# Kernel optimization log

Hardware: AMD Instinct MI355X
Metric: run time of the kernel (lower is better)

Reference implementation:

```python
import jax, jax.numpy as jnp
import numpy as np
from jax import lax

NUM_HEADS = 4
SIDE = 5  # side_dwconv


def setup_inputs() -> dict:
    key = jax.random.key(0)
    ks = jax.random.split(key, 7)
    B, C, H, W = 2, 128, 56, 56
    return {
        "x": jax.random.normal(ks[0], (B, C, H, W), dtype=jnp.float32),
        "qkv_w": jax.random.normal(ks[1], (3 * C, C), dtype=jnp.float32) * 0.02,
        "qkv_b": jax.random.normal(ks[2], (3 * C,), dtype=jnp.float32) * 0.02,
        "lepe_w": jax.random.normal(ks[3], (C, 1, SIDE, SIDE), dtype=jnp.float32) * 0.02,
        "lepe_b": jax.random.normal(ks[4], (C,), dtype=jnp.float32) * 0.02,
        "proj_w": jax.random.normal(ks[5], (C, C), dtype=jnp.float32) * 0.02,
        "proj_b": jax.random.normal(ks[6], (C,), dtype=jnp.float32) * 0.02,
    }


def reference(x, qkv_w, qkv_b, lepe_w, lepe_b, proj_w, proj_b):
    B, C, H, W = x.shape
    nh = NUM_HEADS
    hd = C // nh
    scale = hd ** (-0.5)
    N = H * W

    # 1x1 conv qkv == channel matmul
    qkv = jnp.einsum('oc,bchw->bohw', qkv_w, x) + qkv_b[None, :, None, None]
    q, k, v = jnp.split(qkv, 3, axis=1)  # each [B, C, H, W]

    qr = q.reshape(B, nh, hd, N)
    kr = k.reshape(B, nh, hd, N)
    vr = v.reshape(B, nh, hd, N)

    # attn = q^T k over head_dim -> [B, nh, N, N]
    attn = jnp.einsum('bhdn,bhdm->bhnm', qr, kr) * scale
    attn = jax.nn.softmax(attn, axis=-1)

    # out = attn @ v^T, then permute back to [B, C, H, W]
    out = jnp.einsum('bhnm,bhdm->bhdn', attn, vr).reshape(B, C, H, W)

    # depthwise LePE conv on v, fused with residual add
    pad = SIDE // 2
    lepe = lax.conv_general_dilated(
        v, lepe_w, window_strides=(1, 1), padding=[(pad, pad), (pad, pad)],
        dimension_numbers=('NCHW', 'OIHW', 'NCHW'), feature_group_count=C,
    ) + lepe_b[None, :, None, None]
    out = out + lepe

    # 1x1 conv proj
    out = jnp.einsum('oc,bchw->bohw', proj_w, out) + proj_b[None, :, None, None]
    return out
```

## Files before the change

kernel.cpp:

```cpp
#include <hip/hip_runtime.h>

typedef __bf16 bf16x8 __attribute__((ext_vector_type(8)));
typedef __bf16 bf16x4 __attribute__((ext_vector_type(4)));
typedef float  f32x4  __attribute__((ext_vector_type(4)));

#define NPIX  3136
#define WIMG  56
#define CCH   128
#define NH    4
#define HD    32
#define QSCALE 0.2550565470841439f

#if __has_builtin(__builtin_amdgcn_exp2f)
#define FEXP2(x) __builtin_amdgcn_exp2f(x)
#else
#define FEXP2(x) __expf((x) * 0.6931471805599453f)
#endif


__global__ __launch_bounds__(256) void k_qkv(
    const float* __restrict__ x, const float* __restrict__ qkv_w,
    const float* __restrict__ qkv_b,
    __bf16* __restrict__ qT, __bf16* __restrict__ kT,
    __bf16* __restrict__ vT, __bf16* __restrict__ vP)
{
    __shared__ __bf16 xl[CCH][68];
    const int tid = threadIdx.x;
    const int w = tid >> 6, lane = tid & 63;
    const int col = lane & 15, g = lane >> 4;
    const int px0 = blockIdx.x * 64;
    const int oslab = blockIdx.y;
    const int b = blockIdx.z;
    const int obase = oslab * 64 + w * 16;

    {
        const int pxg = tid & 15, cb = tid >> 4;
        const float* xp = x + (size_t)b * CCH * NPIX + px0 + 4 * pxg;
        #pragma unroll
        for (int pass = 0; pass < 8; ++pass) {
            const int c = cb + 16 * pass;
            const float4 xv = *(const float4*)(xp + (size_t)c * NPIX);
            bf16x4 v = {(__bf16)xv.x, (__bf16)xv.y, (__bf16)xv.z, (__bf16)xv.w};
            *(bf16x4*)&xl[c][4 * pxg] = v;
        }
    }
    __syncthreads();

    f32x4 acc[4];
    #pragma unroll
    for (int a = 0; a < 4; ++a) acc[a] = (f32x4){0.f, 0.f, 0.f, 0.f};

    const float* wrow = qkv_w + (size_t)(obase + col) * CCH;
    #pragma unroll
    for (int ks = 0; ks < 4; ++ks) {
        const int c0 = ks * 32 + g * 8;
        bf16x8 af;
        #pragma unroll
        for (int j = 0; j < 8; ++j) af[j] = (__bf16)wrow[c0 + j];
        #pragma unroll
        for (int a = 0; a < 4; ++a) {
            bf16x8 bf_;
            #pragma unroll
            for (int j = 0; j < 8; ++j) bf_[j] = xl[c0 + j][16 * a + col];
            acc[a] = __builtin_amdgcn_mfma_f32_16x16x32_bf16(af, bf_, acc[a], 0, 0, 0);
        }
    }

    const int orow = obase + g * 4;
    const f32x4 bias4 = *(const f32x4*)(qkv_b + orow);

    if (oslab < 2) {
        const int h = orow >> 5, d0 = orow & 31;
        __bf16* dst = qT + ((size_t)(b * NH + h) * NPIX) * HD + d0;
        #pragma unroll
        for (int a = 0; a < 4; ++a) {
            const int px = px0 + 16 * a + col;
            bf16x4 v;
            #pragma unroll
            for (int r = 0; r < 4; ++r) v[r] = (__bf16)((acc[a][r] + bias4[r]) * QSCALE);
            *(bf16x4*)(dst + (size_t)px * HD) = v;
        }
    } else if (oslab < 4) {
        const int o2 = orow - 128;
        const int h = o2 >> 5, d0 = o2 & 31;
        __bf16* dst = kT + ((size_t)(b * NH + h) * NPIX) * HD + d0;
        #pragma unroll
        for (int a = 0; a < 4; ++a) {
            const int px = px0 + 16 * a + col;
            bf16x4 v;
            #pragma unroll
            for (int r = 0; r < 4; ++r) v[r] = (__bf16)(acc[a][r] + bias4[r]);
            *(bf16x4*)(dst + (size_t)px * HD) = v;
        }
    } else {
        const int c = orow - 256;
        #pragma unroll
        for (int a = 0; a < 4; ++a) {
            const int px = px0 + 16 * a + col;
            bf16x4 v;
            #pragma unroll
            for (int r = 0; r < 4; ++r) v[r] = (__bf16)(acc[a][r] + bias4[r]);
            *(bf16x4*)(vT + ((size_t)(b * NPIX + px)) * CCH + c) = v;
            const int sp = px0 + 4 * col + a;
            #pragma unroll
            for (int r = 0; r < 4; ++r)
                vP[((size_t)(b * CCH + c + r)) * NPIX + sp] = v[r];
        }
    }
}

__global__ __launch_bounds__(256) void k_attn(
    const __bf16* __restrict__ qT, const __bf16* __restrict__ kT,
    const __bf16* __restrict__ vP, const __bf16* __restrict__ vT,
    const float* __restrict__ lepe_w, const float* __restrict__ lepe_b,
    __bf16* __restrict__ attnT)
{
    __shared__ __bf16 P[4][32][72];
    __shared__ float  Opart[4][32][33];
    __shared__ float  lpart[4][32];
    __shared__ float  wl[32][25];
    __shared__ float  bl[32];

    const int tid = threadIdx.x;
    const int w = tid >> 6, lane = tid & 63;
    const int col = lane & 15, g = lane >> 4;
    const int bh = blockIdx.y, b = bh >> 2, h = bh & 3;
    const int qbase = blockIdx.x * 32;
    const size_t headoff = (size_t)bh * NPIX * HD;
    const int c0h = h * HD;

    for (int i = tid; i < 800; i += 256) ((float*)wl)[i] = lepe_w[c0h * 25 + i];
    if (tid < 32) bl[tid] = lepe_b[c0h + tid];

    const bf16x8 aqA = *(const bf16x8*)(qT + headoff + (size_t)(qbase + col) * HD + g * 8);
    const bf16x8 aqB = *(const bf16x8*)(qT + headoff + (size_t)(qbase + 16 + col) * HD + g * 8);

    f32x4 O[2][2];
    #pragma unroll
    for (int i = 0; i < 2; ++i)
        #pragma unroll
        for (int j = 0; j < 2; ++j) O[i][j] = (f32x4){0.f, 0.f, 0.f, 0.f};
    float lacc[2][4] = {{0.f,0.f,0.f,0.f},{0.f,0.f,0.f,0.f}};

    const __bf16* kTh   = kT + headoff;
    const __bf16* vrow0 = vP + (size_t)(b * CCH + c0h + col)      * NPIX;
    const __bf16* vrow1 = vP + (size_t)(b * CCH + c0h + 16 + col) * NPIX;

    const int cs = (49 * w) >> 2, ce = (49 * (w + 1)) >> 2;

#define LOADKV(DK, DV, KK) do { const int _k0 = (KK);                                     \
        _Pragma("unroll")                                                                 \
        for (int _c = 0; _c < 4; ++_c)                                                    \
            DK[_c] = *(const bf16x8*)(kTh + (size_t)(_k0 + 16 * _c + col) * HD + g * 8);  \
        DV[0] = *(const bf16x8*)(vrow0 + _k0      + g * 8);                               \
        DV[1] = *(const bf16x8*)(vrow0 + _k0 + 32 + g * 8);                               \
        DV[2] = *(const bf16x8*)(vrow1 + _k0      + g * 8);                               \
        DV[3] = *(const bf16x8*)(vrow1 + _k0 + 32 + g * 8); } while (0)

    auto compute = [&](const bf16x8* bk, const bf16x8* bv) {
        const f32x4 z = {0.f, 0.f, 0.f, 0.f};
        #pragma unroll
        for (int qh = 0; qh < 2; ++qh) {
            const bf16x8 aq = qh ? aqB : aqA;
            f32x4 s0 = __builtin_amdgcn_mfma_f32_16x16x32_bf16(aq, bk[0], z, 0, 0, 0);
            f32x4 s1 = __builtin_amdgcn_mfma_f32_16x16x32_bf16(aq, bk[1], z, 0, 0, 0);
            f32x4 s2 = __builtin_amdgcn_mfma_f32_16x16x32_bf16(aq, bk[2], z, 0, 0, 0);
            f32x4 s3 = __builtin_amdgcn_mfma_f32_16x16x32_bf16(aq, bk[3], z, 0, 0, 0);
            #pragma unroll
            for (int r = 0; r < 4; ++r) {
                const float p0 = FEXP2(s0[r]), p1 = FEXP2(s1[r]);
                const float p2 = FEXP2(s2[r]), p3 = FEXP2(s3[r]);
                lacc[qh][r] += (p0 + p1) + (p2 + p3);
                bf16x4 pv = {(__bf16)p0, (__bf16)p1, (__bf16)p2, (__bf16)p3};
                *(bf16x4*)&P[w][qh * 16 + g * 4 + r][4 * col] = pv;
            }
        }
        #pragma unroll
        for (int qh = 0; qh < 2; ++qh) {
            const bf16x8 ap0 = *(const bf16x8*)&P[w][qh * 16 + col][g * 8];
            const bf16x8 ap1 = *(const bf16x8*)&P[w][qh * 16 + col][32 + g * 8];
            O[qh][0] = __builtin_amdgcn_mfma_f32_16x16x32_bf16(ap0, bv[0], O[qh][0], 0, 0, 0);
            O[qh][0] = __builtin_amdgcn_mfma_f32_16x16x32_bf16(ap1, bv[1], O[qh][0], 0, 0, 0);
            O[qh][1] = __builtin_amdgcn_mfma_f32_16x16x32_bf16(ap0, bv[2], O[qh][1], 0, 0, 0);
            O[qh][1] = __builtin_amdgcn_mfma_f32_16x16x32_bf16(ap1, bv[3], O[qh][1], 0, 0, 0);
        }
    };

    bf16x8 kA[4], vA[4], kB[4], vBb[4];
    LOADKV(kA, vA, cs * 64);
    int cc = cs;
    while (cc + 2 <= ce) {
        LOADKV(kB, vBb, (cc + 1) * 64);
        compute(kA, vA);
        const int kn = (cc + 2 < ce) ? (cc + 2) * 64 : cs * 64;
        LOADKV(kA, vA, kn);
        compute(kB, vBb);
        cc += 2;
    }
    if (cc < ce) compute(kA, vA);
#undef LOADKV

    #pragma unroll
    for (int qh = 0; qh < 2; ++qh)
        #pragma unroll
        for (int r = 0; r < 4; ++r) {
            float l = lacc[qh][r];
            l += __shfl_xor(l, 1);  l += __shfl_xor(l, 2);
            l += __shfl_xor(l, 4);  l += __shfl_xor(l, 8);
            if (col == 0) lpart[w][qh * 16 + g * 4 + r] = l;
        }
    #pragma unroll
    for (int qh = 0; qh < 2; ++qh)
        #pragma unroll
        for (int r = 0; r < 4; ++r) {
            Opart[w][qh * 16 + g * 4 + r][col]      = O[qh][0][r];
            Opart[w][qh * 16 + g * 4 + r][col + 16] = O[qh][1][r];
        }
    __syncthreads();

    const int q  = tid >> 3;
    const int dq = (tid & 7) * 4;
    const int px = qbase + q;
    const float linv = 1.0f / (lpart[0][q] + lpart[1][q] + lpart[2][q] + lpart[3][q]);
    float o[4];
    #pragma unroll
    for (int i = 0; i < 4; ++i)
        o[i] = (Opart[0][q][dq + i] + Opart[1][q][dq + i] +
                Opart[2][q][dq + i] + Opart[3][q][dq + i]) * linv + bl[dq + i];

    const int py = px / WIMG, pxx = px % WIMG;
    const __bf16* vtb = vT + ((size_t)b * NPIX) * CCH + c0h + dq;
    #pragma unroll
    for (int dy = 0; dy < 5; ++dy) {
        const int yy = py + dy - 2;
        if (yy < 0 || yy >= WIMG) continue;
        #pragma unroll
        for (int dx = 0; dx < 5; ++dx) {
            const int xx = pxx + dx - 2;
            if (xx < 0 || xx >= WIMG) continue;
            const bf16x4 vv = *(const bf16x4*)(vtb + (size_t)(yy * WIMG + xx) * CCH);
            const int tap = dy * 5 + dx;
            #pragma unroll
            for (int i = 0; i < 4; ++i) o[i] += (float)vv[i] * wl[dq + i][tap];
        }
    }
    bf16x4 ov = {(__bf16)o[0], (__bf16)o[1], (__bf16)o[2], (__bf16)o[3]};
    *(bf16x4*)(attnT + ((size_t)(b * NPIX + px)) * CCH + c0h + dq) = ov;
}

__global__ __launch_bounds__(256) void k_proj(
    const __bf16* __restrict__ attnT, const float* __restrict__ proj_w,
    const float* __restrict__ proj_b, float* __restrict__ out)
{
    const int tid = threadIdx.x;
    const int w = tid >> 6, lane = tid & 63;
    const int col = lane & 15, g = lane >> 4;
    const int px0 = blockIdx.x * 32;
    const int obase = blockIdx.y * 64 + w * 16;
    const int b = blockIdx.z;

    const float* wrow = proj_w + (size_t)(obase + col) * CCH;
    const __bf16* abase = attnT + (size_t)(b * NPIX + px0) * CCH;

    f32x4 acc[2];
    acc[0] = (f32x4){0.f, 0.f, 0.f, 0.f};
    acc[1] = (f32x4){0.f, 0.f, 0.f, 0.f};

    #pragma unroll
    for (int ks = 0; ks < 4; ++ks) {
        const int c0 = ks * 32 + g * 8;
        bf16x8 af;
        #pragma unroll
        for (int j = 0; j < 8; ++j) af[j] = (__bf16)wrow[c0 + j];
        #pragma unroll
        for (int a = 0; a < 2; ++a) {
            const bf16x8 bf_ = *(const bf16x8*)(abase + (size_t)(16 * a + col) * CCH + c0);
            acc[a] = __builtin_amdgcn_mfma_f32_16x16x32_bf16(af, bf_, acc[a], 0, 0, 0);
        }
    }

    const f32x4 pb = *(const f32x4*)(proj_b + obase + g * 4);
    #pragma unroll
    for (int a = 0; a < 2; ++a)
        #pragma unroll
        for (int r = 0; r < 4; ++r)
            out[(size_t)(b * CCH + obase + g * 4 + r) * NPIX + px0 + 16 * a + col] =
                acc[a][r] + pb[r];
}

extern "C" void kernel_launch(void* const* d_in, const int* in_sizes, int n_in,
                              void* d_out, int out_size, void* d_ws, size_t ws_size,
                              hipStream_t stream)
{
    const float* x      = (const float*)d_in[0];
    const float* qkv_w  = (const float*)d_in[1];
    const float* qkv_b  = (const float*)d_in[2];
    const float* lepe_w = (const float*)d_in[3];
    const float* lepe_b = (const float*)d_in[4];
    const float* proj_w = (const float*)d_in[5];
    const float* proj_b = (const float*)d_in[6];
    float* out = (float*)d_out;

    char* p = (char*)d_ws;
    __bf16* qT = (__bf16*)p;    p += (size_t)2 * NH * NPIX * HD * 2;
    __bf16* kT = (__bf16*)p;    p += (size_t)2 * NH * NPIX * HD * 2;
    __bf16* vT = (__bf16*)p;    p += (size_t)2 * NPIX * CCH * 2;
    __bf16* vP = (__bf16*)p;    p += (size_t)2 * CCH * NPIX * 2;
    __bf16* attnT = (__bf16*)p;

    k_qkv <<<dim3(49, 6, 2), dim3(256), 0, stream>>>(x, qkv_w, qkv_b, qT, kT, vT, vP);
    k_attn<<<dim3(98, 8),    dim3(256), 0, stream>>>(qT, kT, vP, vT, lepe_w, lepe_b, attnT);
    k_proj<<<dim3(98, 2, 2), dim3(256), 0, stream>>>(attnT, proj_w, proj_b, out);
}
```

Before: 133.7 us.

## Use 8 waves per attention block, transpose qkv LDS tile, retile projection

The attention kernel goes from 4 to 8 waves per block, splitting the key range into eighths. The Opart reduction buffer now aliases the P scratch after a barrier, and V loads are issued inside compute instead of being double-buffered. The qkv kernel stores its x tile pixel-major so MFMA operands come from one 16-byte LDS read, and weights are loaded as float4. The projection kernel is retiled so each wave computes a single 16x16 output tile across twice as many blocks. The aim is more parallelism and occupancy on the dominant attention kernel, at the cost of more partial-sum reduction and less V-load latency hiding.

```diff
diff --git a/kernel.cpp b/kernel.cpp
--- a/kernel.cpp
+++ b/kernel.cpp
@@ -2,6 +2,7 @@
 
 typedef __bf16 bf16x8 __attribute__((ext_vector_type(8)));
 typedef __bf16 bf16x4 __attribute__((ext_vector_type(4)));
+typedef __bf16 bf16x2 __attribute__((ext_vector_type(2)));
 typedef float  f32x4  __attribute__((ext_vector_type(4)));
 
 #define NPIX  3136
@@ -24,7 +25,7 @@
     __bf16* __restrict__ qT, __bf16* __restrict__ kT,
     __bf16* __restrict__ vT, __bf16* __restrict__ vP)
 {
-    __shared__ __bf16 xl[CCH][68];
+    __shared__ __bf16 xl[64][136];
     const int tid = threadIdx.x;
     const int w = tid >> 6, lane = tid & 63;
     const int col = lane & 15, g = lane >> 4;
@@ -34,14 +35,17 @@
     const int obase = oslab * 64 + w * 16;
 
     {
-        const int pxg = tid & 15, cb = tid >> 4;
-        const float* xp = x + (size_t)b * CCH * NPIX + px0 + 4 * pxg;
-        #pragma unroll
-        for (int pass = 0; pass < 8; ++pass) {
-            const int c = cb + 16 * pass;
-            const float4 xv = *(const float4*)(xp + (size_t)c * NPIX);
-            bf16x4 v = {(__bf16)xv.x, (__bf16)xv.y, (__bf16)xv.z, (__bf16)xv.w};
-            *(bf16x4*)&xl[c][4 * pxg] = v;
+        const int px = tid & 63, cq = tid >> 6;
+        const float* xp = x + (size_t)b * CCH * NPIX + px0 + px;
+        #pragma unroll
+        for (int i = 0; i < 8; ++i) {
+            const int c0 = cq * 4 + i * 16;
+            const float v0 = xp[(size_t)(c0 + 0) * NPIX];
+            const float v1 = xp[(size_t)(c0 + 1) * NPIX];
+            const float v2 = xp[(size_t)(c0 + 2) * NPIX];
+            const float v3 = xp[(size_t)(c0 + 3) * NPIX];
+            bf16x4 bv = {(__bf16)v0, (__bf16)v1, (__bf16)v2, (__bf16)v3};
+            *(bf16x4*)&xl[px][c0] = bv;
         }
     }
     __syncthreads();
@@ -54,14 +58,13 @@
     #pragma unroll
     for (int ks = 0; ks < 4; ++ks) {
         const int c0 = ks * 32 + g * 8;
-        bf16x8 af;
-        #pragma unroll
-        for (int j = 0; j < 8; ++j) af[j] = (__bf16)wrow[c0 + j];
+        const float4 wA = *(const float4*)(wrow + c0);
+        const float4 wB = *(const float4*)(wrow + c0 + 4);
+        bf16x8 af = {(__bf16)wA.x, (__bf16)wA.y, (__bf16)wA.z, (__bf16)wA.w,
+                     (__bf16)wB.x, (__bf16)wB.y, (__bf16)wB.z, (__bf16)wB.w};
         #pragma unroll
         for (int a = 0; a < 4; ++a) {
-            bf16x8 bf_;
-            #pragma unroll
-            for (int j = 0; j < 8; ++j) bf_[j] = xl[c0 + j][16 * a + col];
+            const bf16x8 bf_ = *(const bf16x8*)&xl[16 * a + col][c0];
             acc[a] = __builtin_amdgcn_mfma_f32_16x16x32_bf16(af, bf_, acc[a], 0, 0, 0);
         }
     }
@@ -109,15 +112,14 @@
     }
 }
 
-__global__ __launch_bounds__(256) void k_attn(
+__global__ __launch_bounds__(512) void k_attn(
     const __bf16* __restrict__ qT, const __bf16* __restrict__ kT,
     const __bf16* __restrict__ vP, const __bf16* __restrict__ vT,
     const float* __restrict__ lepe_w, const float* __restrict__ lepe_b,
     __bf16* __restrict__ attnT)
 {
-    __shared__ __bf16 P[4][32][72];
-    __shared__ float  Opart[4][32][33];
-    __shared__ float  lpart[4][32];
+    __shared__ __bf16 P[8][32][72];
+    __shared__ float  lpart[8][32];
     __shared__ float  wl[32][25];
     __shared__ float  bl[32];
 
@@ -129,7 +131,7 @@
     const size_t headoff = (size_t)bh * NPIX * HD;
     const int c0h = h * HD;
 
-    for (int i = tid; i < 800; i += 256) ((float*)wl)[i] = lepe_w[c0h * 25 + i];
+    for (int i = tid; i < 800; i += 512) ((float*)wl)[i] = lepe_w[c0h * 25 + i];
     if (tid < 32) bl[tid] = lepe_b[c0h + tid];
 
     const bf16x8 aqA = *(const bf16x8*)(qT + headoff + (size_t)(qbase + col) * HD + g * 8);
@@ -146,18 +148,19 @@
     const __bf16* vrow0 = vP + (size_t)(b * CCH + c0h + col)      * NPIX;
     const __bf16* vrow1 = vP + (size_t)(b * CCH + c0h + 16 + col) * NPIX;
 
-    const int cs = (49 * w) >> 2, ce = (49 * (w + 1)) >> 2;
-
-#define LOADKV(DK, DV, KK) do { const int _k0 = (KK);                                     \
+    const int cs = (49 * w) >> 3, ce = (49 * (w + 1)) >> 3;
+
+#define LOADK(DK, KK) do { const int _k0 = (KK);                                          \
         _Pragma("unroll")                                                                 \
         for (int _c = 0; _c < 4; ++_c)                                                    \
             DK[_c] = *(const bf16x8*)(kTh + (size_t)(_k0 + 16 * _c + col) * HD + g * 8);  \
-        DV[0] = *(const bf16x8*)(vrow0 + _k0      + g * 8);                               \
-        DV[1] = *(const bf16x8*)(vrow0 + _k0 + 32 + g * 8);                               \
-        DV[2] = *(const bf16x8*)(vrow1 + _k0      + g * 8);                               \
-        DV[3] = *(const bf16x8*)(vrow1 + _k0 + 32 + g * 8); } while (0)
-
-    auto compute = [&](const bf16x8* bk, const bf16x8* bv) {
+        } while (0)
+
+    auto compute = [&](const bf16x8* bk, int k0) {
+        const bf16x8 bv0 = *(const bf16x8*)(vrow0 + k0      + g * 8);
+        const bf16x8 bv1 = *(const bf16x8*)(vrow0 + k0 + 32 + g * 8);
+        const bf16x8 bv2 = *(const bf16x8*)(vrow1 + k0      + g * 8);
+        const bf16x8 bv3 = *(const bf16x8*)(vrow1 + k0 + 32 + g * 8);
         const f32x4 z = {0.f, 0.f, 0.f, 0.f};
         #pragma unroll
         for (int qh = 0; qh < 2; ++qh) {
@@ -179,26 +182,25 @@
         for (int qh = 0; qh < 2; ++qh) {
             const bf16x8 ap0 = *(const bf16x8*)&P[w][qh * 16 + col][g * 8];
             const bf16x8 ap1 = *(const bf16x8*)&P[w][qh * 16 + col][32 + g * 8];
-            O[qh][0] = __builtin_amdgcn_mfma_f32_16x16x32_bf16(ap0, bv[0], O[qh][0], 0, 0, 0);
-            O[qh][0] = __builtin_amdgcn_mfma_f32_16x16x32_bf16(ap1, bv[1], O[qh][0], 0, 0, 0);
-            O[qh][1] = __builtin_amdgcn_mfma_f32_16x16x32_bf16(ap0, bv[2], O[qh][1], 0, 0, 0);
-            O[qh][1] = __builtin_amdgcn_mfma_f32_16x16x32_bf16(ap1, bv[3], O[qh][1], 0, 0, 0);
+            O[qh][0] = __builtin_amdgcn_mfma_f32_16x16x32_bf16(ap0, bv0, O[qh][0], 0, 0, 0);
+            O[qh][0] = __builtin_amdgcn_mfma_f32_16x16x32_bf16(ap1, bv1, O[qh][0], 0, 0, 0);
+            O[qh][1] = __builtin_amdgcn_mfma_f32_16x16x32_bf16(ap0, bv2, O[qh][1], 0, 0, 0);
+            O[qh][1] = __builtin_amdgcn_mfma_f32_16x16x32_bf16(ap1, bv3, O[qh][1], 0, 0, 0);
         }
     };
 
-    bf16x8 kA[4], vA[4], kB[4], vBb[4];
-    LOADKV(kA, vA, cs * 64);
+    bf16x8 kA[4], kB[4];
+    LOADK(kA, cs * 64);
     int cc = cs;
     while (cc + 2 <= ce) {
-        LOADKV(kB, vBb, (cc + 1) * 64);
-        compute(kA, vA);
-        const int kn = (cc + 2 < ce) ? (cc + 2) * 64 : cs * 64;
-        LOADKV(kA, vA, kn);
-        compute(kB, vBb);
+        LOADK(kB, (cc + 1) * 64);
+        compute(kA, cc * 64);
+        LOADK(kA, ((cc + 2 < ce) ? cc + 2 : cs) * 64);
+        compute(kB, (cc + 1) * 64);
         cc += 2;
     }
-    if (cc < ce) compute(kA, vA);
-#undef LOADKV
+    if (cc < ce) compute(kA, cc * 64);
+#undef LOADK
 
     #pragma unroll
     for (int qh = 0; qh < 2; ++qh)
@@ -209,6 +211,9 @@
             l += __shfl_xor(l, 4);  l += __shfl_xor(l, 8);
             if (col == 0) lpart[w][qh * 16 + g * 4 + r] = l;
         }
+
+    __syncthreads();
+    float (*Opart)[32][33] = (float(*)[32][33])(&P[0][0][0]);
     #pragma unroll
     for (int qh = 0; qh < 2; ++qh)
         #pragma unroll
@@ -218,18 +223,22 @@
         }
     __syncthreads();
 
-    const int q  = tid >> 3;
-    const int dq = (tid & 7) * 4;
+    const int q  = tid >> 4;
+    const int d2 = (tid & 15) * 2;
     const int px = qbase + q;
-    const float linv = 1.0f / (lpart[0][q] + lpart[1][q] + lpart[2][q] + lpart[3][q]);
-    float o[4];
-    #pragma unroll
-    for (int i = 0; i < 4; ++i)
-        o[i] = (Opart[0][q][dq + i] + Opart[1][q][dq + i] +
-                Opart[2][q][dq + i] + Opart[3][q][dq + i]) * linv + bl[dq + i];
+    float lt = 0.f, o0 = 0.f, o1 = 0.f;
+    #pragma unroll
+    for (int ww = 0; ww < 8; ++ww) {
+        lt += lpart[ww][q];
+        o0 += Opart[ww][q][d2];
+        o1 += Opart[ww][q][d2 + 1];
+    }
+    const float linv = 1.0f / lt;
+    o0 = o0 * linv + bl[d2];
+    o1 = o1 * linv + bl[d2 + 1];
 
     const int py = px / WIMG, pxx = px % WIMG;
-    const __bf16* vtb = vT + ((size_t)b * NPIX) * CCH + c0h + dq;
+    const __bf16* vtb = vT + ((size_t)b * NPIX) * CCH + c0h + d2;
     #pragma unroll
     for (int dy = 0; dy < 5; ++dy) {
         const int yy = py + dy - 2;
@@ -238,14 +247,14 @@
         for (int dx = 0; dx < 5; ++dx) {
             const int xx = pxx + dx - 2;
             if (xx < 0 || xx >= WIMG) continue;
-            const bf16x4 vv = *(const bf16x4*)(vtb + (size_t)(yy * WIMG + xx) * CCH);
+            const bf16x2 vv = *(const bf16x2*)(vtb + (size_t)(yy * WIMG + xx) * CCH);
             const int tap = dy * 5 + dx;
-            #pragma unroll
-            for (int i = 0; i < 4; ++i) o[i] += (float)vv[i] * wl[dq + i][tap];
-        }
-    }
-    bf16x4 ov = {(__bf16)o[0], (__bf16)o[1], (__bf16)o[2], (__bf16)o[3]};
-    *(bf16x4*)(attnT + ((size_t)(b * NPIX + px)) * CCH + c0h + dq) = ov;
+            o0 += (float)vv[0] * wl[d2][tap];
+            o1 += (float)vv[1] * wl[d2 + 1][tap];
+        }
+    }
+    bf16x2 ov = {(__bf16)o0, (__bf16)o1};
+    *(bf16x2*)(attnT + ((size_t)(b * NPIX + px)) * CCH + c0h + d2) = ov;
 }
 
 __global__ __launch_bounds__(256) void k_proj(
@@ -255,37 +264,29 @@
     const int tid = threadIdx.x;
     const int w = tid >> 6, lane = tid & 63;
     const int col = lane & 15, g = lane >> 4;
-    const int px0 = blockIdx.x * 32;
-    const int obase = blockIdx.y * 64 + w * 16;
+    const int px0 = blockIdx.x * 32 + (w >> 1) * 16;
+    const int obase = blockIdx.y * 32 + (w & 1) * 16;
     const int b = blockIdx.z;
 
     const float* wrow = proj_w + (size_t)(obase + col) * CCH;
     const __bf16* abase = attnT + (size_t)(b * NPIX + px0) * CCH;
 
-    f32x4 acc[2];
-    acc[0] = (f32x4){0.f, 0.f, 0.f, 0.f};
-    acc[1] = (f32x4){0.f, 0.f, 0.f, 0.f};
-
+    f32x4 acc = {0.f, 0.f, 0.f, 0.f};
     #pragma unroll
     for (int ks = 0; ks < 4; ++ks) {
         const int c0 = ks * 32 + g * 8;
-        bf16x8 af;
-        #pragma unroll
-        for (int j = 0; j < 8; ++j) af[j] = (__bf16)wrow[c0 + j];
-        #pragma unroll
-        for (int a = 0; a < 2; ++a) {
-            const bf16x8 bf_ = *(const bf16x8*)(abase + (size_t)(16 * a + col) * CCH + c0);
-            acc[a] = __builtin_amdgcn_mfma_f32_16x16x32_bf16(af, bf_, acc[a], 0, 0, 0);
-        }
+        const float4 wA = *(const float4*)(wrow + c0);
+        const float4 wB = *(const float4*)(wrow + c0 + 4);
+        bf16x8 af = {(__bf16)wA.x, (__bf16)wA.y, (__bf16)wA.z, (__bf16)wA.w,
+                     (__bf16)wB.x, (__bf16)wB.y, (__bf16)wB.z, (__bf16)wB.w};
+        const bf16x8 bf_ = *(const bf16x8*)(abase + (size_t)col * CCH + c0);
+        acc = __builtin_amdgcn_mfma_f32_16x16x32_bf16(af, bf_, acc, 0, 0, 0);
     }
 
     const f32x4 pb = *(const f32x4*)(proj_b + obase + g * 4);
     #pragma unroll
-    for (int a = 0; a < 2; ++a)
-        #pragma unroll
-        for (int r = 0; r < 4; ++r)
-            out[(size_t)(b * CCH + obase + g * 4 + r) * NPIX + px0 + 16 * a + col] =
-                acc[a][r] + pb[r];
+    for (int r = 0; r < 4; ++r)
+        out[(size_t)(b * CCH + obase + g * 4 + r) * NPIX + px0 + col] = acc[r] + pb[r];
 }
 
 extern "C" void kernel_launch(void* const* d_in, const int* in_sizes, int n_in,
@@ -309,6 +310,6 @@
     __bf16* attnT = (__bf16*)p;
 
     k_qkv <<<dim3(49, 6, 2), dim3(256), 0, stream>>>(x, qkv_w, qkv_b, qT, kT, vT, vP);
-    k_attn<<<dim3(98, 8),    dim3(256), 0, stream>>>(qT, kT, vP, vT, lepe_w, lepe_b, attnT);
-    k_proj<<<dim3(98, 2, 2), dim3(256), 0, stream>>>(attnT, proj_w, proj_b, out);
+    k_attn<<<dim3(98, 8),    dim3(512), 0, stream>>>(qT, kT, vP, vT, lepe_w, lepe_b, attnT);
+    k_proj<<<dim3(98, 4, 2), dim3(256), 0, stream>>>(attnT, proj_w, proj_b, out);
 }
```

Measured after the change: 149.5 us. 11.8% more time.
